# Performance work log

Hardware: AMD Instinct MI355X
Metric: run time of the kernel (lower is better)

## Reference

```python
import jax, jax.numpy as jnp
import numpy as np

N, E, FIN, H, F = 50000, 800000, 256, 8, 32


def setup_inputs() -> dict:
    key = jax.random.key(0)
    ks = jax.random.split(key, 7)
    x = jax.random.normal(ks[0], (N, FIN), dtype=jnp.float32)
    edge_index = jax.random.randint(ks[1], (2, E), 0, N, dtype=jnp.int64)
    # Glorot-ish scaled params
    W = jax.random.normal(ks[2], (FIN, H * F), dtype=jnp.float32) * (1.0 / np.sqrt(FIN))
    a_src = jax.random.normal(ks[3], (H, F), dtype=jnp.float32) * 0.1
    a_trg = jax.random.normal(ks[4], (H, F), dtype=jnp.float32) * 0.1
    skip_W = jax.random.normal(ks[5], (FIN, H * F), dtype=jnp.float32) * (1.0 / np.sqrt(FIN))
    bias = jnp.zeros((H * F,), dtype=jnp.float32)
    return {"x": x, "edge_index": edge_index, "W": W, "a_src": a_src,
            "a_trg": a_trg, "skip_W": skip_W, "bias": bias}


def reference(x, edge_index, W, a_src, a_trg, skip_W, bias):
    num_nodes = x.shape[0]
    src, trg = edge_index[0], edge_index[1]

    # linear projection  (N, H, F)
    proj = (x @ W).reshape(num_nodes, H, F)

    # per-node attention logits  (N, H)
    scores_source = jnp.einsum('nhf,hf->nh', proj, a_src)
    scores_target = jnp.einsum('nhf,hf->nh', proj, a_trg)

    # lift to edges and score  (E, H)
    scores_per_edge = jax.nn.leaky_relu(scores_source[src] + scores_target[trg],
                                        negative_slope=0.2)
    # global-max subtraction (as in original), then segment softmax over target
    scores_per_edge = scores_per_edge - jnp.max(scores_per_edge)
    exp_scores = jnp.exp(scores_per_edge)
    denom = jax.ops.segment_sum(exp_scores, trg, num_segments=num_nodes)  # (N, H)
    att = exp_scores / (denom[trg] + 1e-16)  # (E, H)

    # weighted aggregation  (N, H, F)
    weighted = proj[src] * att[:, :, None]
    out = jax.ops.segment_sum(weighted, trg, num_segments=num_nodes)

    # skip connection (F != FIN -> projected skip)
    out = out + (x @ skip_W).reshape(num_nodes, H, F)

    # concat heads + bias + ELU
    out = out.reshape(num_nodes, H * F) + bias
    return jax.nn.elu(out)
```

## Files before the change

### kernel.cpp

```cpp
#include <hip/hip_runtime.h>
#include <hip/hip_bf16.h>

#define FIN   256
#define HF    256
#define NCOL  512
#define HEADS 8
#define FDIM  32
#define L2E   1.44269504f
#define BCAP  64
#define NBB   256
#define BK    64

typedef float f32x4 __attribute__((ext_vector_type(4)));
typedef __bf16 bf16x8 __attribute__((ext_vector_type(8)));
typedef unsigned short u16x8 __attribute__((ext_vector_type(8)));

__device__ __forceinline__ unsigned short f2bf(float f) {
  unsigned u = __float_as_uint(f);
  u = u + 0x7FFFu + ((u >> 16) & 1u);
  return (unsigned short)(u >> 16);
}
__device__ __forceinline__ float bf2f(unsigned short s) {
  return __uint_as_float(((unsigned)s) << 16);
}
__device__ __forceinline__ unsigned cvt_pk_bf16(float a, float b) {
  unsigned r;
  asm("v_cvt_pk_bf16_f32 %0, %1, %2" : "=v"(r) : "v"(a), "v"(b));
  return r;
}
__device__ __forceinline__ void gload_lds16(const unsigned short* g, unsigned short* l) {
  __builtin_amdgcn_global_load_lds(
      (const __attribute__((address_space(1))) void*)g,
      (__attribute__((address_space(3))) void*)l,
      16, 0, 0);
}

__global__ void k_prep(const float* __restrict__ W, const float* __restrict__ SW,
                       unsigned short* __restrict__ WT) {
  int tid = blockIdx.x * 256 + threadIdx.x;
  int c = tid >> 8, k = tid & 255;
  float v = (c < HF) ? W[(size_t)k * HF + c] : SW[(size_t)k * HF + (c - HF)];
  WT[(size_t)c * FIN + k] = f2bf(v);
}

__global__ __launch_bounds__(512, 2) void k_gemm(const float* __restrict__ X,
                                                 const unsigned short* __restrict__ WT,
                                                 const float* __restrict__ a_src,
                                                 const float* __restrict__ a_trg,
                                                 unsigned short* __restrict__ Pb,
                                                 float* __restrict__ ss,
                                                 float* __restrict__ st, int Nn,
                                                 const int* __restrict__ eidx,
                                                 int* __restrict__ cnt,
                                                 int* __restrict__ bucket,
                                                 int E, int gblocks) {
  __shared__ __align__(16) unsigned short As[128 * BK];
  __shared__ __align__(16) unsigned short Bs[512 * BK];
  if (blockIdx.x >= gblocks) {
    for (int e = (blockIdx.x - gblocks) * 512 + threadIdx.x; e < E; e += NBB * 512) {
      int trg = eidx[E + e];
      int pos = atomicAdd(&cnt[trg], 1);
      if (pos < BCAP) bucket[((unsigned)trg << 6) + pos] = eidx[e];
    }
    return;
  }
  const int t = threadIdx.x;
  const int bm0 = blockIdx.x * 128;
  const int lane = t & 63, wid = t >> 6;
  const int wm = wid >> 2, wn = wid & 3;
  const int lo = lane & 15, g = lane >> 4;
  const int rsw = lo & 7;
  f32x4 acc[4][8];
#pragma unroll
  for (int i = 0; i < 4; ++i)
#pragma unroll
    for (int j = 0; j < 8; ++j) acc[i][j] = (f32x4){0.f, 0.f, 0.f, 0.f};

  const int arow = t >> 2, ak = t & 3;
  const int aq0 = (2 * ak)     ^ (arow & 7);
  const int aq1 = (2 * ak + 1) ^ (arow & 7);
  int grow = bm0 + arow; if (grow > Nn - 1) grow = Nn - 1;
  const float* xsrc = X + (size_t)grow * FIN + ak * 16;
  const int brow = lane >> 3;
  const int bksg = (lane & 7) ^ (brow & 7);

  float4 f0 = *(const float4*)(xsrc);
  float4 f1 = *(const float4*)(xsrc + 4);
  float4 f2 = *(const float4*)(xsrc + 8);
  float4 f3 = *(const float4*)(xsrc + 12);

  for (int kk = 0; kk < FIN; kk += BK) {
#pragma unroll
    for (int j = 0; j < 8; ++j) {
      int col = wid * 64 + j * 8 + brow;
      const unsigned short* gp = WT + (size_t)col * FIN + kk + bksg * 8;
      gload_lds16(gp, Bs + (wid * 64 + j * 8) * BK);
    }
    uint4 ap0 = {cvt_pk_bf16(f0.x, f0.y), cvt_pk_bf16(f0.z, f0.w),
                 cvt_pk_bf16(f1.x, f1.y), cvt_pk_bf16(f1.z, f1.w)};
    uint4 ap1 = {cvt_pk_bf16(f2.x, f2.y), cvt_pk_bf16(f2.z, f2.w),
                 cvt_pk_bf16(f3.x, f3.y), cvt_pk_bf16(f3.z, f3.w)};
    *(uint4*)(As + arow * BK + aq0 * 8) = ap0;
    *(uint4*)(As + arow * BK + aq1 * 8) = ap1;
    if (kk + BK < FIN) {
      f0 = *(const float4*)(xsrc + kk + BK);
      f1 = *(const float4*)(xsrc + kk + BK + 4);
      f2 = *(const float4*)(xsrc + kk + BK + 8);
      f3 = *(const float4*)(xsrc + kk + BK + 12);
    }
    __syncthreads();
#pragma unroll
    for (int ks = 0; ks < 2; ++ks) {
      bf16x8 a[4], b[8];
#pragma unroll
      for (int mi = 0; mi < 4; ++mi) {
        int row = wm * 64 + mi * 16 + lo;
        a[mi] = __builtin_bit_cast(bf16x8,
            *(const u16x8*)(As + row * BK + (((ks * 4 + g) ^ rsw) * 8)));
      }
#pragma unroll
      for (int ni = 0; ni < 8; ++ni) {
        int col = wn * 128 + ni * 16 + lo;
        b[ni] = __builtin_bit_cast(bf16x8,
            *(const u16x8*)(Bs + col * BK + (((ks * 4 + g) ^ rsw) * 8)));
      }
#pragma unroll
      for (int mi = 0; mi < 4; ++mi)
#pragma unroll
        for (int ni = 0; ni < 8; ++ni)
          acc[mi][ni] = __builtin_amdgcn_mfma_f32_16x16x32_bf16(b[ni], a[mi], acc[mi][ni], 0, 0, 0);
    }
    __syncthreads();
  }
#pragma unroll
  for (int mi = 0; mi < 4; ++mi) {
    int gr = bm0 + wm * 64 + mi * 16 + lo;
    if (gr < Nn) {
#pragma unroll
      for (int ni = 0; ni < 8; ++ni) {
        f32x4 v = acc[mi][ni];
        uint2 pk = {cvt_pk_bf16(v[0], v[1]), cvt_pk_bf16(v[2], v[3])};
        *(uint2*)(Pb + (size_t)gr * NCOL + wn * 128 + ni * 16 + g * 4) = pk;
      }
    }
  }
  if (wn < 2) {
    float psS[4][4], psT[4][4];
#pragma unroll
    for (int mi = 0; mi < 4; ++mi)
#pragma unroll
      for (int hd = 0; hd < 4; ++hd) { psS[mi][hd] = 0.f; psT[mi][hd] = 0.f; }
    const int cbase = wn * 128 + g * 4;
#pragma unroll
    for (int ni = 0; ni < 8; ++ni) {
      float4 av = *(const float4*)(a_src + cbase + ni * 16);
      float4 tv = *(const float4*)(a_trg + cbase + ni * 16);
      int hd = ni >> 1;
#pragma unroll
      for (int mi = 0; mi < 4; ++mi) {
        f32x4 v = acc[mi][ni];
        psS[mi][hd] += v[0]*av.x + v[1]*av.y + v[2]*av.z + v[3]*av.w;
        psT[mi][hd] += v[0]*tv.x + v[1]*tv.y + v[2]*tv.z + v[3]*tv.w;
      }
    }
#pragma unroll
    for (int mi = 0; mi < 4; ++mi) {
      int gr = bm0 + wm * 64 + mi * 16 + lo;
#pragma unroll
      for (int hd = 0; hd < 4; ++hd) {
        float s = psS[mi][hd]; s += __shfl_xor(s, 16); s += __shfl_xor(s, 32);
        float tt = psT[mi][hd]; tt += __shfl_xor(tt, 16); tt += __shfl_xor(tt, 32);
        if (g == hd && gr < Nn) {
          ss[(size_t)gr * 8 + wn * 4 + hd] = s * L2E;
          st[(size_t)gr * 8 + wn * 4 + hd] = tt * L2E;
        }
      }
    }
  }
}

__global__ __launch_bounds__(256) void k_agg(const unsigned short* __restrict__ Pb,
    const int* __restrict__ cnt, const int* __restrict__ bucket,
    const float* __restrict__ ss, const float* __restrict__ st,
    const float* __restrict__ bias, float* __restrict__ out, int Nn) {
  int n = blockIdx.x * 4 + (threadIdx.x >> 6);
  if (n >= Nn) return;
  const int l = threadIdx.x & 63;
  const int h = l >> 3;
  const float sth = st[(unsigned)n * 8 + h];
  float a0 = 0.f, a1 = 0.f, a2 = 0.f, a3 = 0.f, dsum = 0.f;
  int cn = cnt[n]; if (cn > BCAP) cn = BCAP;
  const int* bk = bucket + ((unsigned)n << 6);
  int i = 0;
  for (; i + 1 < cn; i += 2) {
    int s0 = bk[i], s1 = bk[i + 1];
    float v0 = ss[((unsigned)s0 << 3) + h];
    float v1 = ss[((unsigned)s1 << 3) + h];
    ushort4 p0 = *(const ushort4*)(Pb + ((unsigned)s0 << 9) + (l << 2));
    ushort4 p1 = *(const ushort4*)(Pb + ((unsigned)s1 << 9) + (l << 2));
    float x0 = v0 + sth; x0 = fmaxf(x0, 0.2f * x0);
    float x1 = v1 + sth; x1 = fmaxf(x1, 0.2f * x1);
    float w0 = __builtin_amdgcn_exp2f(x0);
    float w1 = __builtin_amdgcn_exp2f(x1);
    dsum += w0 + w1;
    a0 += w0 * bf2f(p0.x) + w1 * bf2f(p1.x);
    a1 += w0 * bf2f(p0.y) + w1 * bf2f(p1.y);
    a2 += w0 * bf2f(p0.z) + w1 * bf2f(p1.z);
    a3 += w0 * bf2f(p0.w) + w1 * bf2f(p1.w);
  }
  if (i < cn) {
    int s0 = bk[i];
    float v0 = ss[((unsigned)s0 << 3) + h];
    ushort4 p0 = *(const ushort4*)(Pb + ((unsigned)s0 << 9) + (l << 2));
    float x0 = v0 + sth; x0 = fmaxf(x0, 0.2f * x0);
    float w0 = __builtin_amdgcn_exp2f(x0);
    dsum += w0;
    a0 += w0 * bf2f(p0.x); a1 += w0 * bf2f(p0.y);
    a2 += w0 * bf2f(p0.z); a3 += w0 * bf2f(p0.w);
  }
  float inv = 1.f / (dsum + 1e-16f);
  ushort4 sk = *(const ushort4*)(Pb + ((unsigned)n << 9) + HF + (l << 2));
  float4 bi = *(const float4*)(bias + (l << 2));
  float o0 = a0 * inv + bf2f(sk.x) + bi.x;
  float o1 = a1 * inv + bf2f(sk.y) + bi.y;
  float o2 = a2 * inv + bf2f(sk.z) + bi.z;
  float o3 = a3 * inv + bf2f(sk.w) + bi.w;
  o0 = o0 > 0.f ? o0 : expm1f(o0);
  o1 = o1 > 0.f ? o1 : expm1f(o1);
  o2 = o2 > 0.f ? o2 : expm1f(o2);
  o3 = o3 > 0.f ? o3 : expm1f(o3);
  float4 o = {o0, o1, o2, o3};
  *(float4*)(out + ((unsigned)n << 8) + (l << 2)) = o;
}

extern "C" void kernel_launch(void* const* d_in, const int* in_sizes, int n_in,
                              void* d_out, int out_size, void* d_ws, size_t ws_size,
                              hipStream_t stream) {
  const float* x      = (const float*)d_in[0];
  const int*   eidx   = (const int*)d_in[1];
  const float* W      = (const float*)d_in[2];
  const float* a_src  = (const float*)d_in[3];
  const float* a_trg  = (const float*)d_in[4];
  const float* skip_W = (const float*)d_in[5];
  const float* bias   = (const float*)d_in[6];
  float* out = (float*)d_out;
  const int Nn = in_sizes[0] / FIN;
  const int E  = in_sizes[1] / 2;

  char* p = (char*)d_ws;
  auto carve = [&](size_t bytes) { char* r = p; p += (bytes + 255) & ~(size_t)255; return r; };
  unsigned short* WT = (unsigned short*)carve((size_t)NCOL * FIN * 2);
  unsigned short* Pb = (unsigned short*)carve((size_t)Nn * NCOL * 2);
  float* ss   = (float*)carve((size_t)Nn * HEADS * 4);
  float* st   = (float*)carve((size_t)Nn * HEADS * 4);
  int* cnt    = (int*)carve((size_t)Nn * 4);
  int* bucket = (int*)carve((size_t)Nn * BCAP * 4);

  hipMemsetAsync(cnt, 0, (size_t)Nn * 4, stream);

  hipLaunchKernelGGL(k_prep, dim3((NCOL * FIN) / 256), dim3(256), 0, stream,
                     W, skip_W, WT);
  const int gblocks = (Nn + 127) / 128;
  hipLaunchKernelGGL(k_gemm, dim3(gblocks + NBB), dim3(512), 0, stream,
                     x, WT, a_src, a_trg, Pb, ss, st, Nn,
                     eidx, cnt, bucket, E, gblocks);
  hipLaunchKernelGGL(k_agg, dim3((Nn + 3) / 4), dim3(256), 0, stream,
                     Pb, cnt, bucket, ss, st, bias, out, Nn);
}
```

Before: 150.3 us.

## Split GEMM output columns across two 256-thread blocks per row tile

The projection GEMM now uses 256-thread blocks, each computing a 128x256 output tile, with two blocks per 128-row tile. That halves the B tile in LDS and doubles the number of blocks, aiming for better occupancy and more even CU load. The X register prefetch across k-steps is dropped in favour of direct loads inside the loop, and each X row is read and converted to bf16 twice, once per column block. Attention score computation is restricted to the bn0==0 block, and the edge-bucketing blocks are resized to 256 threads.

```diff
diff --git a/kernel.cpp b/kernel.cpp
--- a/kernel.cpp
+++ b/kernel.cpp
@@ -43,7 +43,7 @@
   WT[(size_t)c * FIN + k] = f2bf(v);
 }
 
-__global__ __launch_bounds__(512, 2) void k_gemm(const float* __restrict__ X,
+__global__ __launch_bounds__(256, 2) void k_gemm(const float* __restrict__ X,
                                                  const unsigned short* __restrict__ WT,
                                                  const float* __restrict__ a_src,
                                                  const float* __restrict__ a_trg,
@@ -53,11 +53,11 @@
                                                  const int* __restrict__ eidx,
                                                  int* __restrict__ cnt,
                                                  int* __restrict__ bucket,
-                                                 int E, int gblocks) {
+                                                 int E, int gblocks2) {
   __shared__ __align__(16) unsigned short As[128 * BK];
-  __shared__ __align__(16) unsigned short Bs[512 * BK];
-  if (blockIdx.x >= gblocks) {
-    for (int e = (blockIdx.x - gblocks) * 512 + threadIdx.x; e < E; e += NBB * 512) {
+  __shared__ __align__(16) unsigned short Bs[256 * BK];
+  if (blockIdx.x >= gblocks2) {
+    for (int e = (blockIdx.x - gblocks2) * 256 + threadIdx.x; e < E; e += NBB * 256) {
       int trg = eidx[E + e];
       int pos = atomicAdd(&cnt[trg], 1);
       if (pos < BCAP) bucket[((unsigned)trg << 6) + pos] = eidx[e];
@@ -65,9 +65,10 @@
     return;
   }
   const int t = threadIdx.x;
-  const int bm0 = blockIdx.x * 128;
+  const int bm0 = (blockIdx.x >> 1) * 128;
+  const int bn0 = (blockIdx.x & 1) * 256;
   const int lane = t & 63, wid = t >> 6;
-  const int wm = wid >> 2, wn = wid & 3;
+  const int wm = wid >> 1, wn = wid & 1;
   const int lo = lane & 15, g = lane >> 4;
   const int rsw = lo & 7;
   f32x4 acc[4][8];
@@ -76,37 +77,28 @@
 #pragma unroll
     for (int j = 0; j < 8; ++j) acc[i][j] = (f32x4){0.f, 0.f, 0.f, 0.f};
 
-  const int arow = t >> 2, ak = t & 3;
-  const int aq0 = (2 * ak)     ^ (arow & 7);
-  const int aq1 = (2 * ak + 1) ^ (arow & 7);
+  const int arow = t >> 1, ah = t & 1;
   int grow = bm0 + arow; if (grow > Nn - 1) grow = Nn - 1;
-  const float* xsrc = X + (size_t)grow * FIN + ak * 16;
+  const float* xsrc = X + (size_t)grow * FIN + ah * 32;
+  const int arx = arow & 7;
   const int brow = lane >> 3;
-  const int bksg = (lane & 7) ^ (brow & 7);
-
-  float4 f0 = *(const float4*)(xsrc);
-  float4 f1 = *(const float4*)(xsrc + 4);
-  float4 f2 = *(const float4*)(xsrc + 8);
-  float4 f3 = *(const float4*)(xsrc + 12);
+  const int bksg = (lane & 7) ^ brow;
 
   for (int kk = 0; kk < FIN; kk += BK) {
 #pragma unroll
     for (int j = 0; j < 8; ++j) {
-      int col = wid * 64 + j * 8 + brow;
+      int col = bn0 + wid * 64 + j * 8 + brow;
       const unsigned short* gp = WT + (size_t)col * FIN + kk + bksg * 8;
       gload_lds16(gp, Bs + (wid * 64 + j * 8) * BK);
     }
-    uint4 ap0 = {cvt_pk_bf16(f0.x, f0.y), cvt_pk_bf16(f0.z, f0.w),
-                 cvt_pk_bf16(f1.x, f1.y), cvt_pk_bf16(f1.z, f1.w)};
-    uint4 ap1 = {cvt_pk_bf16(f2.x, f2.y), cvt_pk_bf16(f2.z, f2.w),
-                 cvt_pk_bf16(f3.x, f3.y), cvt_pk_bf16(f3.z, f3.w)};
-    *(uint4*)(As + arow * BK + aq0 * 8) = ap0;
-    *(uint4*)(As + arow * BK + aq1 * 8) = ap1;
-    if (kk + BK < FIN) {
-      f0 = *(const float4*)(xsrc + kk + BK);
-      f1 = *(const float4*)(xsrc + kk + BK + 4);
-      f2 = *(const float4*)(xsrc + kk + BK + 8);
-      f3 = *(const float4*)(xsrc + kk + BK + 12);
+#pragma unroll
+    for (int q = 0; q < 4; ++q) {
+      float4 u0 = *(const float4*)(xsrc + kk + q * 8);
+      float4 u1 = *(const float4*)(xsrc + kk + q * 8 + 4);
+      uint4 pk = {cvt_pk_bf16(u0.x, u0.y), cvt_pk_bf16(u0.z, u0.w),
+                  cvt_pk_bf16(u1.x, u1.y), cvt_pk_bf16(u1.z, u1.w)};
+      int qq = (ah * 4 + q) ^ arx;
+      *(uint4*)(As + arow * BK + qq * 8) = pk;
     }
     __syncthreads();
 #pragma unroll
@@ -140,11 +132,11 @@
       for (int ni = 0; ni < 8; ++ni) {
         f32x4 v = acc[mi][ni];
         uint2 pk = {cvt_pk_bf16(v[0], v[1]), cvt_pk_bf16(v[2], v[3])};
-        *(uint2*)(Pb + (size_t)gr * NCOL + wn * 128 + ni * 16 + g * 4) = pk;
-      }
-    }
-  }
-  if (wn < 2) {
+        *(uint2*)(Pb + (size_t)gr * NCOL + bn0 + wn * 128 + ni * 16 + g * 4) = pk;
+      }
+    }
+  }
+  if (bn0 == 0) {
     float psS[4][4], psT[4][4];
 #pragma unroll
     for (int mi = 0; mi < 4; ++mi)
@@ -260,10 +252,10 @@
 
   hipLaunchKernelGGL(k_prep, dim3((NCOL * FIN) / 256), dim3(256), 0, stream,
                      W, skip_W, WT);
-  const int gblocks = (Nn + 127) / 128;
-  hipLaunchKernelGGL(k_gemm, dim3(gblocks + NBB), dim3(512), 0, stream,
+  const int gblocks2 = ((Nn + 127) / 128) * 2;
+  hipLaunchKernelGGL(k_gemm, dim3(gblocks2 + NBB), dim3(256), 0, stream,
                      x, WT, a_src, a_trg, Pb, ss, st, Nn,
-                     eidx, cnt, bucket, E, gblocks);
+                     eidx, cnt, bucket, E, gblocks2);
   hipLaunchKernelGGL(k_agg, dim3((Nn + 3) / 4), dim3(256), 0, stream,
                      Pb, cnt, bucket, ss, st, bias, out, Nn);
 }
```

Result: slower. 164.2 us (+9.2%).
